# Optimization experiments

Hardware: AMD Instinct MI355X
Metric: run time of the kernel (lower is better)

The kernel has to match this reference:

```python
import jax, jax.numpy as jnp
import numpy as np

N = 16384
E = 524288
IN_DIM = 128
LATENT = 48
EPS = 1e-5


def setup_inputs() -> dict:
    key = jax.random.key(0)
    ks = jax.random.split(key, 20)
    def rn(k, shape, scale=0.05):
        return jax.random.normal(k, shape, dtype=jnp.float32) * scale
    return {
        "x": jax.random.normal(ks[0], (N, IN_DIM), dtype=jnp.float32),
        "edge_index": jax.random.randint(ks[1], (2, E), 0, N, dtype=jnp.int64),
        "W1": rn(ks[2], (IN_DIM, 256)), "b1": jnp.zeros((256,), jnp.float32),
        "W2": rn(ks[3], (256, 128)),    "b2": jnp.zeros((128,), jnp.float32),
        "W3": rn(ks[4], (128, LATENT)), "b3": jnp.zeros((LATENT,), jnp.float32),
        "skip_W": rn(ks[5], (IN_DIM, LATENT)), "skip_b": jnp.zeros((LATENT,), jnp.float32),
        "bn_gamma": jnp.ones((256,), jnp.float32), "bn_beta": jnp.zeros((256,), jnp.float32),
        "bn_mean": rn(ks[6], (256,), 0.01), "bn_var": jnp.ones((256,), jnp.float32),
        "dpW1": rn(ks[7], (LATENT, 64)), "dpb1": jnp.zeros((64,), jnp.float32),
        "dpW2": rn(ks[8], (64, 1)),      "dpb2": jnp.zeros((1,), jnp.float32),
    }


def _gcn_norm(edge_index, n):
    # add self-loops, compute symmetric normalization (PyG gcn_norm)
    loops = jnp.arange(n, dtype=edge_index.dtype)
    src = jnp.concatenate([edge_index[0], loops])
    dst = jnp.concatenate([edge_index[1], loops])
    deg = jax.ops.segment_sum(jnp.ones_like(dst, dtype=jnp.float32), dst, num_segments=n)
    dinv = jnp.where(deg > 0, jax.lax.rsqrt(jnp.maximum(deg, 1.0)), 0.0)
    norm = dinv[src] * dinv[dst]  # [E+N]
    return src, dst, norm


def _gcn_conv(x, src, dst, norm, W, b, n):
    h = x @ W                                    # [N, out]
    msg = h[src] * norm[:, None]                 # gather + scale, [E+N, out]
    return jax.ops.segment_sum(msg, dst, num_segments=n) + b


def reference(x, edge_index, W1, b1, W2, b2, W3, b3, skip_W, skip_b,
              bn_gamma, bn_beta, bn_mean, bn_var, dpW1, dpb1, dpW2, dpb2):
    n = x.shape[0]
    src, dst, norm = _gcn_norm(edge_index, n)
    identity = x @ skip_W + skip_b
    h = _gcn_conv(x, src, dst, norm, W1, b1, n)
    # BatchNorm1d (inference mode: running stats), then ReLU; dropout = identity (eval)
    h = (h - bn_mean) * jax.lax.rsqrt(bn_var + EPS) * bn_gamma + bn_beta
    h = jax.nn.relu(h)
    h = jax.nn.relu(_gcn_conv(h, src, dst, norm, W2, b2, n))
    z = _gcn_conv(h, src, dst, norm, W3, b3, n) + identity   # [N, latent]
    adj_recon = jax.nn.sigmoid(z @ z.T)                      # [N, N]
    degree_pred = (jax.nn.relu(z @ dpW1 + dpb1) @ dpW2 + dpb2).squeeze(-1)
    return z, adj_recon, degree_pred
```

## Files before the change

kernel.cpp:

```cpp
#include <hip/hip_runtime.h>
#include <hip/hip_bf16.h>
#include <math.h>

#define NN   16384
#define EE   524288
#define TOTE (EE + NN)

typedef short s16x8 __attribute__((ext_vector_type(8)));
typedef float f32x16 __attribute__((ext_vector_type(16)));

__device__ inline unsigned short bf16r(float f) {
    unsigned int u = __float_as_uint(f);
    return (unsigned short)((u + 0x7FFFu + ((u >> 16) & 1u)) >> 16);
}

__global__ void k_prep(const float* __restrict__ x,  const float* __restrict__ W1,
                       const float* __restrict__ W2, const float* __restrict__ W3,
                       const float* __restrict__ skW,
                       const float* __restrict__ b1, const float* __restrict__ gamma,
                       const float* __restrict__ beta, const float* __restrict__ mean,
                       const float* __restrict__ var,
                       unsigned short* __restrict__ xb,  unsigned short* __restrict__ W1t,
                       unsigned short* __restrict__ W2t, unsigned short* __restrict__ W3t,
                       unsigned short* __restrict__ skWt,
                       float* __restrict__ bnA, float* __restrict__ bnC,
                       int* __restrict__ deg, int* __restrict__ cur) {
    const int S0 = NN * 128;
    const int S1 = S0 + 256 * 128;
    const int S2 = S1 + 128 * 256;
    const int S3 = S2 + 64 * 128;
    const int S4 = S3 + 64 * 128;
    int i = blockIdx.x * 256 + threadIdx.x;
    if (i < NN) { deg[i] = 0; cur[i] = 0; }
    if (i < S0) { xb[i] = bf16r(x[i]); }
    else if (i < S1) { int j = i - S0; int n = j >> 7, k = j & 127; W1t[j] = bf16r(W1[k * 256 + n]); }
    else if (i < S2) { int j = i - S1; int n = j >> 8, k = j & 255; W2t[j] = bf16r(W2[k * 128 + n]); }
    else if (i < S3) { int j = i - S2; int n = j >> 7, k = j & 127; W3t[j] = (n < 48) ? bf16r(W3[k * 48 + n]) : 0; }
    else if (i < S4) { int j = i - S3; int n = j >> 7, k = j & 127; skWt[j] = (n < 48) ? bf16r(skW[k * 48 + n]) : 0; }
    else if (i < S4 + 256) {
        int j = i - S4;
        float a = gamma[j] * rsqrtf(var[j] + 1e-5f);
        bnA[j] = a;
        bnC[j] = (b1[j] - mean[j]) * a + beta[j];
    }
}

__global__ void k_deg(const int* __restrict__ ei, int* __restrict__ deg) {
    int e = blockIdx.x * blockDim.x + threadIdx.x;
    if (e < EE) atomicAdd(&deg[ei[EE + e]], 1);
}

__global__ __launch_bounds__(1024) void k_scan(const int* __restrict__ deg,
                                               int* __restrict__ off,
                                               float* __restrict__ dinv) {
    __shared__ int part[1024];
    int t = threadIdx.x;
    int base = t * 16;
    int loc[16];
    int s = 0;
#pragma unroll
    for (int q = 0; q < 16; q++) {
        loc[q] = deg[base + q] + 1;
        dinv[base + q] = rsqrtf((float)loc[q]);
        s += loc[q];
    }
    part[t] = s;
    __syncthreads();
    for (int d = 1; d < 1024; d <<= 1) {
        int v = (t >= d) ? part[t - d] : 0;
        __syncthreads();
        part[t] += v;
        __syncthreads();
    }
    int ex = (t == 0) ? 0 : part[t - 1];
#pragma unroll
    for (int q = 0; q < 16; q++) { off[base + q] = ex; ex += loc[q]; }
    if (t == 1023) off[NN] = ex;
}

__global__ void k_fill(const int* __restrict__ ei, const int* __restrict__ off,
                       int* __restrict__ cur, const float* __restrict__ dinv,
                       int* __restrict__ cs, float* __restrict__ cw) {
    int e = blockIdx.x * blockDim.x + threadIdx.x;
    if (e >= TOTE) return;
    int s, d;
    if (e < EE) { s = ei[e]; d = ei[EE + e]; }
    else        { s = d = e - EE; }
    int pos = off[d] + atomicAdd(&cur[d], 1);
    cs[pos] = s;
    cw[pos] = dinv[s] * dinv[d];
}

template <int MODE>
__global__ void k_agg128(const unsigned short* __restrict__ H, const int* __restrict__ off,
                         const int* __restrict__ cs, const float* __restrict__ cw,
                         const float* __restrict__ bias, unsigned short* __restrict__ Y) {
    int node = blockIdx.x * 4 + (threadIdx.x >> 6);
    int lane = threadIdx.x & 63;
    int s0 = off[node], cnt = off[node + 1] - s0;
    const unsigned int* Hp = (const unsigned int*)H;
    float ax = 0.f, ay = 0.f;
    for (int base = 0; base < cnt; base += 64) {
        int nb = cnt - base; if (nb > 64) nb = 64;
        int vi = 0; float vw = 0.f;
        if (lane < nb) { vi = cs[s0 + base + lane]; vw = cw[s0 + base + lane]; }
        int e = 0;
        for (; e + 8 <= nb; e += 8) {
            unsigned int u[8]; float ww[8];
#pragma unroll
            for (int q = 0; q < 8; q++) {
                int   iq = __shfl(vi, e + q);
                ww[q]    = __shfl(vw, e + q);
                u[q] = Hp[(size_t)iq * 64 + lane];
            }
#pragma unroll
            for (int q = 0; q < 8; q++) {
                ax += __uint_as_float(u[q] << 16) * ww[q];
                ay += __uint_as_float(u[q] & 0xffff0000u) * ww[q];
            }
        }
        for (; e < nb; e++) {
            int i0 = __shfl(vi, e); float w0 = __shfl(vw, e);
            unsigned int u0 = Hp[(size_t)i0 * 64 + lane];
            ax += __uint_as_float(u0 << 16) * w0;
            ay += __uint_as_float(u0 & 0xffff0000u) * w0;
        }
    }
    if constexpr (MODE == 2) {
        ax = fmaxf(ax + bias[2 * lane], 0.f);
        ay = fmaxf(ay + bias[2 * lane + 1], 0.f);
    }
    unsigned int o = ((unsigned int)bf16r(ay) << 16) | bf16r(ax);
    ((unsigned int*)Y)[(size_t)node * 64 + lane] = o;
}

__global__ void k_aggz(const float* __restrict__ H, const int* __restrict__ off,
                       const int* __restrict__ cs, const float* __restrict__ cw,
                       const float* __restrict__ b3, const float* __restrict__ idb,
                       const float* __restrict__ dpW1, const float* __restrict__ dpb1,
                       const float* __restrict__ dpW2, const float* __restrict__ dpb2,
                       float* __restrict__ zout, unsigned short* __restrict__ zb,
                       float* __restrict__ dpout) {
    int node = blockIdx.x * 4 + (threadIdx.x >> 6);
    int lane = threadIdx.x & 63;
    int s0 = off[node], cnt = off[node + 1] - s0;
    float a = 0.f;
    for (int base = 0; base < cnt; base += 64) {
        int nb = cnt - base; if (nb > 64) nb = 64;
        int vi = 0; float vw = 0.f;
        if (lane < nb) { vi = cs[s0 + base + lane]; vw = cw[s0 + base + lane]; }
        int e = 0;
        for (; e + 8 <= nb; e += 8) {
            float v[8], ww[8];
#pragma unroll
            for (int q = 0; q < 8; q++) {
                int   iq = __shfl(vi, e + q);
                ww[q]    = __shfl(vw, e + q);
                v[q] = (lane < 48) ? H[(size_t)iq * 64 + lane] : 0.f;
            }
#pragma unroll
            for (int q = 0; q < 8; q++) a += v[q] * ww[q];
        }
        for (; e < nb; e++) {
            int i0 = __shfl(vi, e); float w0 = __shfl(vw, e);
            if (lane < 48) a += H[(size_t)i0 * 64 + lane] * w0;
        }
    }
    float zv = 0.f;
    if (lane < 48) {
        zv = a + b3[lane] + idb[(size_t)node * 64 + lane];
        zout[(size_t)node * 48 + lane] = zv;
        zb[(size_t)node * 48 + lane] = bf16r(zv);
    }
    float hj = dpb1[lane];
#pragma unroll
    for (int k = 0; k < 48; k++) hj += __shfl(zv, k) * dpW1[k * 64 + lane];
    hj = fmaxf(hj, 0.f);
    float p = hj * dpW2[lane];
    for (int o = 32; o > 0; o >>= 1) p += __shfl_down(p, o);
    if (lane == 0) dpout[node] = p + dpb2[0];
}

template <int K, int NP, int MODE, int TW>
__global__ void k_mm(const unsigned short* __restrict__ A,
                     const unsigned short* __restrict__ Bt,
                     const float* __restrict__ P0, const float* __restrict__ P1,
                     void* __restrict__ Yv) {
    int wv = threadIdx.x >> 6, l = threadIdx.x & 63;
    int ti = blockIdx.x;
    int tj = blockIdx.y * TW + wv;
    int r = l & 31, hi = l >> 5;
    const s16x8* ap = (const s16x8*)(A + (size_t)(ti * 32 + r) * K + 8 * hi);
    const s16x8* bp = (const s16x8*)(Bt + (size_t)(tj * 32 + r) * K + 8 * hi);
    f32x16 c = {};
#pragma unroll
    for (int kk = 0; kk < K / 16; kk++)
        c = __builtin_amdgcn_mfma_f32_32x32x16_bf16(ap[2 * kk], bp[2 * kk], c, 0, 0, 0);
    int col = tj * 32 + r;
#pragma unroll
    for (int reg = 0; reg < 16; reg++) {
        int row = ti * 32 + (reg & 3) + 8 * (reg >> 2) + 4 * hi;
        float v = c[reg];
        if constexpr (MODE == 1) {
            v = fmaxf(v * P0[col] + P1[col], 0.f);
            ((unsigned short*)Yv)[(size_t)row * NP + col] = bf16r(v);
        } else if constexpr (MODE == 0) {
            ((unsigned short*)Yv)[(size_t)row * NP + col] = bf16r(v);
        } else if constexpr (MODE == 2) {
            ((float*)Yv)[(size_t)row * NP + col] = v + P0[col];
        } else {
            ((float*)Yv)[(size_t)row * NP + col] = v;
        }
    }
}

__global__ void k_mm3s(const unsigned short* __restrict__ h2a,
                       const unsigned short* __restrict__ W3t,
                       const unsigned short* __restrict__ xb,
                       const unsigned short* __restrict__ skWt,
                       const float* __restrict__ skb,
                       float* __restrict__ h3, float* __restrict__ idb) {
    int wv = threadIdx.x >> 6, l = threadIdx.x & 63;
    int ti = blockIdx.x;
    int tj = wv;
    int r = l & 31, hi = l >> 5;
    const unsigned short* A  = (blockIdx.y == 0) ? h2a : xb;
    const unsigned short* Bt = (blockIdx.y == 0) ? W3t : skWt;
    const s16x8* ap = (const s16x8*)(A + (size_t)(ti * 32 + r) * 128 + 8 * hi);
    const s16x8* bp = (const s16x8*)(Bt + (size_t)(tj * 32 + r) * 128 + 8 * hi);
    f32x16 c = {};
#pragma unroll
    for (int kk = 0; kk < 8; kk++)
        c = __builtin_amdgcn_mfma_f32_32x32x16_bf16(ap[2 * kk], bp[2 * kk], c, 0, 0, 0);
    int col = tj * 32 + r;
    float add = (blockIdx.y == 0) ? 0.f : ((col < 48) ? skb[col] : 0.f);
    float* Y = (blockIdx.y == 0) ? h3 : idb;
#pragma unroll
    for (int reg = 0; reg < 16; reg++) {
        int row = ti * 32 + (reg & 3) + 8 * (reg >> 2) + 4 * hi;
        Y[(size_t)row * 64 + col] = c[reg] + add;
    }
}

__global__ __launch_bounds__(256) void k_adj2(const unsigned short* __restrict__ zb,
                                              float* __restrict__ out) {
    int wv = threadIdx.x >> 6;
    int l  = threadIdx.x & 63;
    int ti = blockIdx.y;
    int tj = blockIdx.x * 4 + wv;
    int r  = l & 31;
    int hi = l >> 5;

    const s16x8* ap = (const s16x8*)(zb + (size_t)(ti * 32 + r) * 48 + 8 * hi);
    const s16x8* bp = (const s16x8*)(zb + (size_t)(tj * 32 + r) * 48 + 8 * hi);

    f32x16 c = {};
#pragma unroll
    for (int kk = 0; kk < 3; kk++) {
        s16x8 a = ap[2 * kk];
        s16x8 b = bp[2 * kk];
        c = __builtin_amdgcn_mfma_f32_32x32x16_bf16(a, b, c, 0, 0, 0);
    }

    size_t colbase = (size_t)tj * 32 + r;
#pragma unroll
    for (int reg = 0; reg < 16; reg++) {
        int row = ti * 32 + (reg & 3) + 8 * (reg >> 2) + 4 * hi;
        float v = 1.f / (1.f + __expf(-c[reg]));
        __builtin_nontemporal_store(v, out + (size_t)row * NN + colbase);
    }
}

extern "C" void kernel_launch(void* const* d_in, const int* in_sizes, int n_in,
                              void* d_out, int out_size, void* d_ws, size_t ws_size,
                              hipStream_t stream) {
    const float* x      = (const float*)d_in[0];
    const int*   ei     = (const int*)d_in[1];
    const float* W1     = (const float*)d_in[2];
    const float* b1     = (const float*)d_in[3];
    const float* W2     = (const float*)d_in[4];
    const float* b2     = (const float*)d_in[5];
    const float* W3     = (const float*)d_in[6];
    const float* b3     = (const float*)d_in[7];
    const float* skW    = (const float*)d_in[8];
    const float* skb    = (const float*)d_in[9];
    const float* gamma  = (const float*)d_in[10];
    const float* beta   = (const float*)d_in[11];
    const float* mean   = (const float*)d_in[12];
    const float* var    = (const float*)d_in[13];
    const float* dpW1   = (const float*)d_in[14];
    const float* dpb1   = (const float*)d_in[15];
    const float* dpW2   = (const float*)d_in[16];
    const float* dpb2   = (const float*)d_in[17];

    float* zout   = (float*)d_out;
    float* adjout = zout + (size_t)NN * 48;
    float* dpout  = adjout + (size_t)NN * NN;

    char* w = (char*)d_ws;
    auto alloc = [&](size_t bytes) {
        char* p = w; w += ((bytes + 255) & ~(size_t)255); return p;
    };
    int*   deg  = (int*)alloc((size_t)NN * 4);
    int*   cur  = (int*)alloc((size_t)NN * 4);
    int*   off  = (int*)alloc((size_t)(NN + 1) * 4);
    int*   cs   = (int*)alloc((size_t)TOTE * 4);
    float* cw   = (float*)alloc((size_t)TOTE * 4);
    float* dinv = (float*)alloc((size_t)NN * 4);
    float* bnA  = (float*)alloc(256 * 4);
    float* bnC  = (float*)alloc(256 * 4);
    unsigned short* xb   = (unsigned short*)alloc((size_t)NN * 128 * 2);
    unsigned short* W1t  = (unsigned short*)alloc(256 * 128 * 2);
    unsigned short* W2t  = (unsigned short*)alloc(128 * 256 * 2);
    unsigned short* W3t  = (unsigned short*)alloc(64 * 128 * 2);
    unsigned short* skWt = (unsigned short*)alloc(64 * 128 * 2);
    unsigned short* xa   = (unsigned short*)alloc((size_t)NN * 128 * 2);
    unsigned short* h1   = (unsigned short*)alloc((size_t)NN * 256 * 2);
    unsigned short* h2   = (unsigned short*)alloc((size_t)NN * 128 * 2);
    unsigned short* h2a  = (unsigned short*)alloc((size_t)NN * 128 * 2);
    float* h3   = (float*)alloc((size_t)NN * 64 * 4);
    float* idb  = (float*)alloc((size_t)NN * 64 * 4);
    unsigned short* zb = (unsigned short*)alloc((size_t)NN * 48 * 2);

    const int PREP = NN * 128 + 256 * 128 + 128 * 256 + 64 * 128 + 64 * 128 + 256;
    k_prep<<<(PREP + 255) / 256, 256, 0, stream>>>(x, W1, W2, W3, skW,
                                                   b1, gamma, beta, mean, var,
                                                   xb, W1t, W2t, W3t, skWt,
                                                   bnA, bnC, deg, cur);
    k_deg<<<EE / 256, 256, 0, stream>>>(ei, deg);
    k_scan<<<1, 1024, 0, stream>>>(deg, off, dinv);
    k_fill<<<TOTE / 256, 256, 0, stream>>>(ei, off, cur, dinv, cs, cw);

    k_agg128<0><<<NN / 4, 256, 0, stream>>>(xb, off, cs, cw, nullptr, xa);
    k_mm<128, 256, 1, 4><<<dim3(NN / 32, 2), 256, 0, stream>>>(xa, W1t, bnA, bnC, h1);
    k_mm<256, 128, 0, 4><<<dim3(NN / 32, 1), 256, 0, stream>>>(h1, W2t, nullptr, nullptr, h2);
    k_agg128<2><<<NN / 4, 256, 0, stream>>>(h2, off, cs, cw, b2, h2a);
    k_mm3s<<<dim3(NN / 32, 2), 128, 0, stream>>>(h2a, W3t, xb, skWt, skb, h3, idb);
    k_aggz<<<NN / 4, 256, 0, stream>>>(h3, off, cs, cw, b3, idb,
                                       dpW1, dpb1, dpW2, dpb2, zout, zb, dpout);

    k_adj2<<<dim3(128, 512), 256, 0, stream>>>(zb, adjout);
}
```

Before: 324.7 us.

## Factor GCN edge norm into per-node pre/post scaling and fuse degree count into prep

```diff
diff --git a/kernel.cpp b/kernel.cpp
--- a/kernel.cpp
+++ b/kernel.cpp
@@ -19,19 +19,19 @@
                        const float* __restrict__ skW,
                        const float* __restrict__ b1, const float* __restrict__ gamma,
                        const float* __restrict__ beta, const float* __restrict__ mean,
-                       const float* __restrict__ var,
+                       const float* __restrict__ var,  const int* __restrict__ ei,
                        unsigned short* __restrict__ xb,  unsigned short* __restrict__ W1t,
                        unsigned short* __restrict__ W2t, unsigned short* __restrict__ W3t,
                        unsigned short* __restrict__ skWt,
                        float* __restrict__ bnA, float* __restrict__ bnC,
-                       int* __restrict__ deg, int* __restrict__ cur) {
+                       int* __restrict__ deg) {
     const int S0 = NN * 128;
     const int S1 = S0 + 256 * 128;
     const int S2 = S1 + 128 * 256;
     const int S3 = S2 + 64 * 128;
     const int S4 = S3 + 64 * 128;
     int i = blockIdx.x * 256 + threadIdx.x;
-    if (i < NN) { deg[i] = 0; cur[i] = 0; }
+    if (i < EE) atomicAdd(&deg[ei[EE + i]], 1);
     if (i < S0) { xb[i] = bf16r(x[i]); }
     else if (i < S1) { int j = i - S0; int n = j >> 7, k = j & 127; W1t[j] = bf16r(W1[k * 256 + n]); }
     else if (i < S2) { int j = i - S1; int n = j >> 8, k = j & 255; W2t[j] = bf16r(W2[k * 128 + n]); }
@@ -45,16 +45,11 @@
     }
 }
 
-__global__ void k_deg(const int* __restrict__ ei, int* __restrict__ deg) {
-    int e = blockIdx.x * blockDim.x + threadIdx.x;
-    if (e < EE) atomicAdd(&deg[ei[EE + e]], 1);
-}
-
 __global__ __launch_bounds__(1024) void k_scan(const int* __restrict__ deg,
                                                int* __restrict__ off,
                                                float* __restrict__ dinv) {
-    __shared__ int part[1024];
-    int t = threadIdx.x;
+    __shared__ int wsum[16], wex[16];
+    int t = threadIdx.x, lane = t & 63, wid = t >> 6;
     int base = t * 16;
     int loc[16];
     int s = 0;
@@ -64,36 +59,48 @@
         dinv[base + q] = rsqrtf((float)loc[q]);
         s += loc[q];
     }
-    part[t] = s;
+    int incl = s;
+#pragma unroll
+    for (int d = 1; d < 64; d <<= 1) {
+        int v = __shfl_up(incl, d);
+        if (lane >= d) incl += v;
+    }
+    if (lane == 63) wsum[wid] = incl;
     __syncthreads();
-    for (int d = 1; d < 1024; d <<= 1) {
-        int v = (t >= d) ? part[t - d] : 0;
-        __syncthreads();
-        part[t] += v;
-        __syncthreads();
-    }
-    int ex = (t == 0) ? 0 : part[t - 1];
+    if (t < 16) {
+        int v = wsum[t], iv = v;
+#pragma unroll
+        for (int d = 1; d < 16; d <<= 1) {
+            int u = __shfl_up(iv, d);
+            if (t >= d) iv += u;
+        }
+        wex[t] = iv - v;
+    }
+    __syncthreads();
+    int ex = wex[wid] + incl - s;
 #pragma unroll
     for (int q = 0; q < 16; q++) { off[base + q] = ex; ex += loc[q]; }
     if (t == 1023) off[NN] = ex;
 }
 
-__global__ void k_fill(const int* __restrict__ ei, const int* __restrict__ off,
-                       int* __restrict__ cur, const float* __restrict__ dinv,
-                       int* __restrict__ cs, float* __restrict__ cw) {
-    int e = blockIdx.x * blockDim.x + threadIdx.x;
-    if (e >= TOTE) return;
-    int s, d;
-    if (e < EE) { s = ei[e]; d = ei[EE + e]; }
-    else        { s = d = e - EE; }
-    int pos = off[d] + atomicAdd(&cur[d], 1);
-    cs[pos] = s;
-    cw[pos] = dinv[s] * dinv[d];
+__global__ void k_fillx(const int* __restrict__ ei, const int* __restrict__ off,
+                        int* __restrict__ cur, const float* __restrict__ x,
+                        const float* __restrict__ dinv,
+                        int* __restrict__ cs, unsigned short* __restrict__ xbs) {
+    int i = blockIdx.x * 256 + threadIdx.x;
+    if (i < TOTE) {
+        int s, d;
+        if (i < EE) { s = ei[i]; d = ei[EE + i]; }
+        else        { s = d = i - EE; }
+        int pos = off[d] + atomicAdd(&cur[d], 1);
+        cs[pos] = s;
+    }
+    if (i < NN * 128) xbs[i] = bf16r(x[i] * dinv[i >> 7]);
 }
 
 template <int MODE>
 __global__ void k_agg128(const unsigned short* __restrict__ H, const int* __restrict__ off,
-                         const int* __restrict__ cs, const float* __restrict__ cw,
+                         const int* __restrict__ cs, const float* __restrict__ dinv,
                          const float* __restrict__ bias, unsigned short* __restrict__ Y) {
     int node = blockIdx.x * 4 + (threadIdx.x >> 6);
     int lane = threadIdx.x & 63;
@@ -102,30 +109,30 @@
     float ax = 0.f, ay = 0.f;
     for (int base = 0; base < cnt; base += 64) {
         int nb = cnt - base; if (nb > 64) nb = 64;
-        int vi = 0; float vw = 0.f;
-        if (lane < nb) { vi = cs[s0 + base + lane]; vw = cw[s0 + base + lane]; }
+        int vi = (lane < nb) ? cs[s0 + base + lane] : 0;
         int e = 0;
         for (; e + 8 <= nb; e += 8) {
-            unsigned int u[8]; float ww[8];
+            unsigned int u[8];
 #pragma unroll
             for (int q = 0; q < 8; q++) {
-                int   iq = __shfl(vi, e + q);
-                ww[q]    = __shfl(vw, e + q);
+                int iq = __shfl(vi, e + q);
                 u[q] = Hp[(size_t)iq * 64 + lane];
             }
 #pragma unroll
             for (int q = 0; q < 8; q++) {
-                ax += __uint_as_float(u[q] << 16) * ww[q];
-                ay += __uint_as_float(u[q] & 0xffff0000u) * ww[q];
+                ax += __uint_as_float(u[q] << 16);
+                ay += __uint_as_float(u[q] & 0xffff0000u);
             }
         }
         for (; e < nb; e++) {
-            int i0 = __shfl(vi, e); float w0 = __shfl(vw, e);
-            unsigned int u0 = Hp[(size_t)i0 * 64 + lane];
-            ax += __uint_as_float(u0 << 16) * w0;
-            ay += __uint_as_float(u0 & 0xffff0000u) * w0;
-        }
-    }
+            int iq = __shfl(vi, e);
+            unsigned int u0 = Hp[(size_t)iq * 64 + lane];
+            ax += __uint_as_float(u0 << 16);
+            ay += __uint_as_float(u0 & 0xffff0000u);
+        }
+    }
+    float dn = dinv[node];
+    ax *= dn; ay *= dn;
     if constexpr (MODE == 2) {
         ax = fmaxf(ax + bias[2 * lane], 0.f);
         ay = fmaxf(ay + bias[2 * lane + 1], 0.f);
@@ -134,8 +141,8 @@
     ((unsigned int*)Y)[(size_t)node * 64 + lane] = o;
 }
 
-__global__ void k_aggz(const float* __restrict__ H, const int* __restrict__ off,
-                       const int* __restrict__ cs, const float* __restrict__ cw,
+__global__ void k_aggz(const unsigned short* __restrict__ H, const int* __restrict__ off,
+                       const int* __restrict__ cs, const float* __restrict__ dinv,
                        const float* __restrict__ b3, const float* __restrict__ idb,
                        const float* __restrict__ dpW1, const float* __restrict__ dpb1,
                        const float* __restrict__ dpW2, const float* __restrict__ dpb2,
@@ -147,28 +154,26 @@
     float a = 0.f;
     for (int base = 0; base < cnt; base += 64) {
         int nb = cnt - base; if (nb > 64) nb = 64;
-        int vi = 0; float vw = 0.f;
-        if (lane < nb) { vi = cs[s0 + base + lane]; vw = cw[s0 + base + lane]; }
+        int vi = (lane < nb) ? cs[s0 + base + lane] : 0;
         int e = 0;
         for (; e + 8 <= nb; e += 8) {
-            float v[8], ww[8];
+            float v[8];
 #pragma unroll
             for (int q = 0; q < 8; q++) {
-                int   iq = __shfl(vi, e + q);
-                ww[q]    = __shfl(vw, e + q);
-                v[q] = (lane < 48) ? H[(size_t)iq * 64 + lane] : 0.f;
+                int iq = __shfl(vi, e + q);
+                v[q] = __uint_as_float((unsigned int)H[(size_t)iq * 64 + lane] << 16);
             }
 #pragma unroll
-            for (int q = 0; q < 8; q++) a += v[q] * ww[q];
+            for (int q = 0; q < 8; q++) a += v[q];
         }
         for (; e < nb; e++) {
-            int i0 = __shfl(vi, e); float w0 = __shfl(vw, e);
-            if (lane < 48) a += H[(size_t)i0 * 64 + lane] * w0;
+            int iq = __shfl(vi, e);
+            a += __uint_as_float((unsigned int)H[(size_t)iq * 64 + lane] << 16);
         }
     }
     float zv = 0.f;
     if (lane < 48) {
-        zv = a + b3[lane] + idb[(size_t)node * 64 + lane];
+        zv = a * dinv[node] + b3[lane] + idb[(size_t)node * 64 + lane];
         zout[(size_t)node * 48 + lane] = zv;
         zb[(size_t)node * 48 + lane] = bf16r(zv);
     }
@@ -185,6 +190,7 @@
 __global__ void k_mm(const unsigned short* __restrict__ A,
                      const unsigned short* __restrict__ Bt,
                      const float* __restrict__ P0, const float* __restrict__ P1,
+                     const float* __restrict__ RS,
                      void* __restrict__ Yv) {
     int wv = threadIdx.x >> 6, l = threadIdx.x & 63;
     int ti = blockIdx.x;
@@ -204,12 +210,8 @@
         if constexpr (MODE == 1) {
             v = fmaxf(v * P0[col] + P1[col], 0.f);
             ((unsigned short*)Yv)[(size_t)row * NP + col] = bf16r(v);
-        } else if constexpr (MODE == 0) {
-            ((unsigned short*)Yv)[(size_t)row * NP + col] = bf16r(v);
-        } else if constexpr (MODE == 2) {
-            ((float*)Yv)[(size_t)row * NP + col] = v + P0[col];
         } else {
-            ((float*)Yv)[(size_t)row * NP + col] = v;
+            ((unsigned short*)Yv)[(size_t)row * NP + col] = bf16r(v * RS[row]);
         }
     }
 }
@@ -218,8 +220,8 @@
                        const unsigned short* __restrict__ W3t,
                        const unsigned short* __restrict__ xb,
                        const unsigned short* __restrict__ skWt,
-                       const float* __restrict__ skb,
-                       float* __restrict__ h3, float* __restrict__ idb) {
+                       const float* __restrict__ skb, const float* __restrict__ dinv,
+                       unsigned short* __restrict__ h3b, float* __restrict__ idb) {
     int wv = threadIdx.x >> 6, l = threadIdx.x & 63;
     int ti = blockIdx.x;
     int tj = wv;
@@ -233,12 +235,19 @@
     for (int kk = 0; kk < 8; kk++)
         c = __builtin_amdgcn_mfma_f32_32x32x16_bf16(ap[2 * kk], bp[2 * kk], c, 0, 0, 0);
     int col = tj * 32 + r;
-    float add = (blockIdx.y == 0) ? 0.f : ((col < 48) ? skb[col] : 0.f);
-    float* Y = (blockIdx.y == 0) ? h3 : idb;
-#pragma unroll
-    for (int reg = 0; reg < 16; reg++) {
-        int row = ti * 32 + (reg & 3) + 8 * (reg >> 2) + 4 * hi;
-        Y[(size_t)row * 64 + col] = c[reg] + add;
+    if (blockIdx.y == 0) {
+#pragma unroll
+        for (int reg = 0; reg < 16; reg++) {
+            int row = ti * 32 + (reg & 3) + 8 * (reg >> 2) + 4 * hi;
+            h3b[(size_t)row * 64 + col] = bf16r(c[reg] * dinv[row]);
+        }
+    } else {
+        float add = (col < 48) ? skb[col] : 0.f;
+#pragma unroll
+        for (int reg = 0; reg < 16; reg++) {
+            int row = ti * 32 + (reg & 3) + 8 * (reg >> 2) + 4 * hi;
+            idb[(size_t)row * 64 + col] = c[reg] + add;
+        }
     }
 }
 
@@ -305,11 +314,11 @@
     int*   cur  = (int*)alloc((size_t)NN * 4);
     int*   off  = (int*)alloc((size_t)(NN + 1) * 4);
     int*   cs   = (int*)alloc((size_t)TOTE * 4);
-    float* cw   = (float*)alloc((size_t)TOTE * 4);
     float* dinv = (float*)alloc((size_t)NN * 4);
     float* bnA  = (float*)alloc(256 * 4);
     float* bnC  = (float*)alloc(256 * 4);
     unsigned short* xb   = (unsigned short*)alloc((size_t)NN * 128 * 2);
+    unsigned short* xbs  = (unsigned short*)alloc((size_t)NN * 128 * 2);
     unsigned short* W1t  = (unsigned short*)alloc(256 * 128 * 2);
     unsigned short* W2t  = (unsigned short*)alloc(128 * 256 * 2);
     unsigned short* W3t  = (unsigned short*)alloc(64 * 128 * 2);
@@ -318,25 +327,26 @@
     unsigned short* h1   = (unsigned short*)alloc((size_t)NN * 256 * 2);
     unsigned short* h2   = (unsigned short*)alloc((size_t)NN * 128 * 2);
     unsigned short* h2a  = (unsigned short*)alloc((size_t)NN * 128 * 2);
-    float* h3   = (float*)alloc((size_t)NN * 64 * 4);
+    unsigned short* h3b  = (unsigned short*)alloc((size_t)NN * 64 * 2);
     float* idb  = (float*)alloc((size_t)NN * 64 * 4);
     unsigned short* zb = (unsigned short*)alloc((size_t)NN * 48 * 2);
 
+    hipMemsetAsync(deg, 0, (size_t)NN * 8, stream);
+
     const int PREP = NN * 128 + 256 * 128 + 128 * 256 + 64 * 128 + 64 * 128 + 256;
     k_prep<<<(PREP + 255) / 256, 256, 0, stream>>>(x, W1, W2, W3, skW,
-                                                   b1, gamma, beta, mean, var,
+                                                   b1, gamma, beta, mean, var, ei,
                                                    xb, W1t, W2t, W3t, skWt,
-                                                   bnA, bnC, deg, cur);
-    k_deg<<<EE / 256, 256, 0, stream>>>(ei, deg);
+                                                   bnA, bnC, deg);
     k_scan<<<1, 1024, 0, stream>>>(deg, off, dinv);
-    k_fill<<<TOTE / 256, 256, 0, stream>>>(ei, off, cur, dinv, cs, cw);
-
-    k_agg128<0><<<NN / 4, 256, 0, stream>>>(xb, off, cs, cw, nullptr, xa);
-    k_mm<128, 256, 1, 4><<<dim3(NN / 32, 2), 256, 0, stream>>>(xa, W1t, bnA, bnC, h1);
-    k_mm<256, 128, 0, 4><<<dim3(NN / 32, 1), 256, 0, stream>>>(h1, W2t, nullptr, nullptr, h2);
-    k_agg128<2><<<NN / 4, 256, 0, stream>>>(h2, off, cs, cw, b2, h2a);
-    k_mm3s<<<dim3(NN / 32, 2), 128, 0, stream>>>(h2a, W3t, xb, skWt, skb, h3, idb);
-    k_aggz<<<NN / 4, 256, 0, stream>>>(h3, off, cs, cw, b3, idb,
+    k_fillx<<<NN * 128 / 256, 256, 0, stream>>>(ei, off, cur, x, dinv, cs, xbs);
+
+    k_agg128<0><<<NN / 4, 256, 0, stream>>>(xbs, off, cs, dinv, nullptr, xa);
+    k_mm<128, 256, 1, 4><<<dim3(NN / 32, 2), 256, 0, stream>>>(xa, W1t, bnA, bnC, nullptr, h1);
+    k_mm<256, 128, 4, 4><<<dim3(NN / 32, 1), 256, 0, stream>>>(h1, W2t, nullptr, nullptr, dinv, h2);
+    k_agg128<2><<<NN / 4, 256, 0, stream>>>(h2, off, cs, dinv, b2, h2a);
+    k_mm3s<<<dim3(NN / 32, 2), 128, 0, stream>>>(h2a, W3t, xb, skWt, skb, dinv, h3b, idb);
+    k_aggz<<<NN / 4, 256, 0, stream>>>(h3b, off, cs, dinv, b3, idb,
                                        dpW1, dpb1, dpW2, dpb2, zout, zb, dpout);
 
     k_adj2<<<dim3(128, 512), 256, 0, stream>>>(zb, adjout);
```

Result: faster. 315.5 us (-2.8%).
